# Performance work log

Measured on AMD Instinct MI355X. Metric: run time of the kernel, lower is better.

Reference implementation:

```python
import jax, jax.numpy as jnp
import numpy as np

B, N, E, H = 4, 20000, 320000, 5
STEPS = 10


def _linear_init(key, fan_in, fan_out):
    k1, k2 = jax.random.split(key)
    s = 1.0 / np.sqrt(fan_in)
    W = jax.random.uniform(k1, (fan_in, fan_out), minval=-s, maxval=s, dtype=jnp.float32)
    bias = jax.random.uniform(k2, (fan_out,), minval=-s, maxval=s, dtype=jnp.float32)
    return W, bias


def setup_inputs() -> dict:
    key = jax.random.key(0)
    ks = jax.random.split(key, 13)
    inp = {}
    inp['J_msg'] = jax.random.normal(ks[0], (B, E, 1), dtype=jnp.float32)
    inp['b'] = jax.random.normal(ks[1], (B, N, 1), dtype=jnp.float32)
    inp['index_in'] = jax.random.randint(ks[2], (E,), 0, N, dtype=jnp.int32)
    inp['index_out'] = jax.random.randint(ks[3], (E,), 0, N, dtype=jnp.int32)
    # message MLP: (H+4 -> 64 -> 64 -> 5)
    inp['mW1'], inp['mb1'] = _linear_init(ks[4], H + 4, 64)
    inp['mW2'], inp['mb2'] = _linear_init(ks[5], 64, 64)
    inp['mW3'], inp['mb3'] = _linear_init(ks[6], 64, H)
    # GRU gates: (3H -> H)
    inp['gzW'], inp['gzb'] = _linear_init(ks[7], 3 * H, H)
    inp['grW'], inp['grb'] = _linear_init(ks[8], 3 * H, H)
    inp['ghW'], inp['ghb'] = _linear_init(ks[9], 3 * H, H)
    # out head: (H+1 -> 64 -> 64 -> 1)
    inp['oW1'], inp['ob1'] = _linear_init(ks[10], H + 1, 64)
    inp['oW2'], inp['ob2'] = _linear_init(ks[11], 64, 64)
    inp['oW3'], inp['ob3'] = _linear_init(ks[12], 64, 1)
    return inp


def reference(J_msg, b, index_in, index_out,
              mW1, mb1, mW2, mb2, mW3, mb3,
              gzW, gzb, grW, grb, ghW, ghb,
              oW1, ob1, oW2, ob2, oW3, ob3):
    b_in = b[:, index_in]    # [B,E,1]
    b_out = b[:, index_out]  # [B,E,1]

    def message(h_e):  # h_e: [B,E,H]
        x = jnp.concatenate([h_e, b_in, b_out, J_msg, -J_msg], axis=-1)  # [B,E,H+4]
        x = jax.nn.relu(x @ mW1 + mb1)
        x = jax.nn.relu(x @ mW2 + mb2)
        return x @ mW3 + mb3  # [B,E,H]

    h_t_0 = jnp.zeros((B, N, H), dtype=J_msg.dtype)
    h_t_1 = jnp.zeros((B, N, H), dtype=J_msg.dtype)
    m_t_0 = jnp.zeros((B, N, H), dtype=J_msg.dtype)
    m_t_1 = jnp.zeros((B, N, H), dtype=J_msg.dtype)

    for _ in range(STEPS):
        me0 = message(h_t_0[:, index_out])
        me1 = message(h_t_1[:, index_out])
        # faithful to torch source: m_t_0 accumulates across steps,
        # and m_t_1 is built from the UPDATED m_t_0 (repo quirk).
        m_t_0 = m_t_0.at[:, index_out].add(me0)
        m_t_1 = m_t_0.at[:, index_out].add(me1)
        a = jnp.concatenate([h_t_1, m_t_0, m_t_1], axis=-1)  # [B,N,3H]
        z = jax.nn.sigmoid(a @ gzW + gzb)
        r = jax.nn.sigmoid(a @ grW + grb)
        joined = jnp.concatenate([r * h_t_1, m_t_0, m_t_1], axis=-1)
        h_hat = jnp.tanh(joined @ ghW + ghb)
        h_new = (1 - z) * h_t_1 + z * h_hat
        h_t_0 = h_t_1
        h_t_1 = h_new

    x = jnp.concatenate([h_t_1, b], axis=-1)  # [B,N,H+1]
    x = jax.nn.relu(x @ oW1 + ob1)
    x = jax.nn.relu(x @ oW2 + ob2)
    out = jax.nn.sigmoid(x @ oW3 + ob3)  # [B,N,1]
    return out.reshape(B, 1, -1)
```

## Files before the change

kernel.cpp:

```cpp
#include <hip/hip_runtime.h>
#include <hip/hip_bf16.h>
#include <math.h>

#define Hd 5
#define NN 20000
#define EE 320000
#define NBATCH 4
#define BNH (NBATCH * NN * Hd)

typedef __attribute__((ext_vector_type(8))) short short8;
typedef __attribute__((ext_vector_type(4))) float f32x4;
typedef __attribute__((ext_vector_type(4))) unsigned int uint4v;

__device__ __forceinline__ float sigmoidf_(float v) {
    return 1.0f / (1.0f + expf(-v));
}

__device__ __forceinline__ unsigned short bf16bits(float v) {
    __hip_bfloat16 h = __float2bfloat16(v);
    return *(unsigned short*)&h;
}
__device__ __forceinline__ float bf16tof(unsigned short u) {
    __hip_bfloat16 h = *(__hip_bfloat16*)&u;
    return __bfloat162float(h);
}

__global__ void k_hist(const int* __restrict__ iout, unsigned* __restrict__ cnt) {
    int t = blockIdx.x * 256 + threadIdx.x;
    atomicAdd(&cnt[iout[t]], 1u);
}

__global__ void k_scan(const unsigned* __restrict__ cnt, unsigned* __restrict__ row) {
    __shared__ unsigned part[256];
    int i = threadIdx.x;
    unsigned s = 0;
    if (i < 250) {
        for (int k = 0; k < 80; ++k) s += cnt[i * 80 + k];
    }
    part[i] = s;
    __syncthreads();
    for (int off = 1; off < 256; off <<= 1) {
        unsigned v = part[i];
        unsigned u = (i >= off) ? part[i - off] : 0u;
        __syncthreads();
        part[i] = v + u;
        __syncthreads();
    }
    unsigned run = (i == 0) ? 0u : part[i - 1];
    if (i < 250) {
        for (int k = 0; k < 80; ++k) {
            row[i * 80 + k] = run;
            run += cnt[i * 80 + k];
        }
    }
}

__global__ void k_scatter(const int* __restrict__ iout,
                          const unsigned* __restrict__ row,
                          unsigned* __restrict__ cur,
                          unsigned* __restrict__ perm) {
    int t = blockIdx.x * 256 + threadIdx.x;
    int io = iout[t];
    unsigned pos = row[io] + atomicAdd(&cur[io], 1u);
    perm[pos] = (unsigned)t;
}

__global__ void k_mat(const unsigned* __restrict__ perm,
                      const int* __restrict__ iout, const int* __restrict__ iin,
                      const float* __restrict__ Jm,
                      int* __restrict__ sout, int* __restrict__ sin,
                      float* __restrict__ sJ) {
    int t = blockIdx.x * 256 + threadIdx.x;
    unsigned e = perm[t];
    sout[t] = iout[e];
    sin[t]  = iin[e];
#pragma unroll
    for (int b = 0; b < NBATCH; ++b)
        sJ[(size_t)b * EE + t] = Jm[(size_t)b * EE + e];
}

__global__ void k_wfrag(const float* __restrict__ W1, const float* __restrict__ W2,
                        const float* __restrict__ W3,
                        unsigned short* __restrict__ af1,
                        unsigned short* __restrict__ af2,
                        unsigned short* __restrict__ af3) {
    int t = blockIdx.x * 256 + threadIdx.x;
    if (t < 2048) {
        int j  = t & 7;
        int l  = (t >> 3) & 63;
        int qt = t >> 9;
        int g  = l >> 4;
        int q  = qt * 16 + (l & 15);
        float base = (j < 7) ? W1[j * 64 + q] : (W1[7 * 64 + q] - W1[8 * 64 + q]);
        unsigned short w0 = bf16bits(base);
        af1[t] = (g < 2) ? w0 : bf16bits(base - bf16tof(w0));
    }
    if (t < 4096) {
        int j  = t & 7;
        int l  = (t >> 3) & 63;
        int kt = (t >> 9) & 1;
        int qt = t >> 10;
        int g  = l >> 4;
        int p  = l & 15;
        int nk = (j >> 1) * 16 + 4 * g + 2 * kt + (j & 1);
        int no = (qt & 1) * 32 + 8 * (p >> 2) + 4 * (qt >> 1) + (p & 3);
        af2[t] = bf16bits(W2[nk * 64 + no]);
    }
    if (t < 1024) {
        int j  = t & 7;
        int l  = (t >> 3) & 63;
        int kt = t >> 9;
        int i  = l & 15;
        int g3 = l >> 4;
        int n  = kt * 32 + 8 * g3 + j;
        af3[t] = (i < 5) ? bf16bits(W3[n * 5 + i]) : (unsigned short)0;
    }
}

__global__ void __launch_bounds__(256, 2) msg_kernel(
    const float* __restrict__ sJ, const float* __restrict__ bnode,
    const int* __restrict__ sin, const int* __restrict__ sout,
    const float* __restrict__ b1,
    const unsigned short* __restrict__ af1,
    const unsigned short* __restrict__ af2,
    const unsigned short* __restrict__ af3,
    const float* __restrict__ b2, const float* __restrict__ b3,
    const float* __restrict__ h1,
    float* __restrict__ sCur)
{
    int wid  = threadIdx.x >> 6;
    int lane = threadIdx.x & 63;
    int g = lane >> 4;
    int c = lane & 15;
    int E0 = blockIdx.x * 256 + wid * 64;
    int bb = blockIdx.y;
    int e  = E0 + lane;

    int io = sout[e];
    int ii = sin[e];
    size_t hoff = ((size_t)bb * NN + io) * Hd;

    float xf[8];
#pragma unroll
    for (int i = 0; i < Hd; ++i) xf[i] = h1[hoff + i];
    xf[5] = bnode[bb * NN + ii];
    xf[6] = bnode[bb * NN + io];
    xf[7] = sJ[(size_t)bb * EE + e];

    uint4v B1l[4];
#pragma unroll
    for (int et = 0; et < 4; ++et) {
        float xe[8];
#pragma unroll
        for (int f = 0; f < 8; ++f) xe[f] = __shfl(xf[f], et * 16 + c, 64);

        uint4v hiP, loP;
#pragma unroll
        for (int j2 = 0; j2 < 4; ++j2) {
            float va = xe[2 * j2], vb = xe[2 * j2 + 1];
            unsigned ta = __float_as_uint(va), tb = __float_as_uint(vb);
            unsigned ha = ta & 0xFFFF0000u, hb = tb & 0xFFFF0000u;
            hiP[j2] = hb | (ta >> 16);
            float ra = va - __uint_as_float(ha);
            float rb = vb - __uint_as_float(hb);
            unsigned pk;
            asm("v_cvt_pk_bf16_f32 %0, %1, %2" : "=v"(pk) : "v"(ra), "v"(rb));
            loP[j2] = pk;
        }
#pragma unroll
        for (int d = 0; d < 4; ++d) B1l[et][d] = (g & 1) ? loP[d] : hiP[d];
    }

    const short8* pA1 = (const short8*)af1;
    f32x4 D1[4][4];
#pragma unroll
    for (int qt = 0; qt < 4; ++qt) {
        float4 bb1 = *(const float4*)(b1 + qt * 16 + 4 * g);
        short8 a1f = pA1[qt * 64 + lane];
#pragma unroll
        for (int et = 0; et < 4; ++et) {
            f32x4 dinit = (f32x4){bb1.x, bb1.y, bb1.z, bb1.w};
            D1[qt][et] = __builtin_amdgcn_mfma_f32_16x16x32_bf16(
                a1f, __builtin_bit_cast(short8, B1l[et]), dinit, 0, 0, 0);
        }
    }

    short8 B2[4][2];
#pragma unroll
    for (int et = 0; et < 4; ++et) {
        uint4v w0, w1;
#pragma unroll
        for (int qt = 0; qt < 4; ++qt) {
            float r0 = fmaxf(D1[qt][et][0], 0.0f);
            float r1 = fmaxf(D1[qt][et][1], 0.0f);
            float r2 = fmaxf(D1[qt][et][2], 0.0f);
            float r3 = fmaxf(D1[qt][et][3], 0.0f);
            unsigned p0, p1;
            asm("v_cvt_pk_bf16_f32 %0, %1, %2" : "=v"(p0) : "v"(r0), "v"(r1));
            asm("v_cvt_pk_bf16_f32 %0, %1, %2" : "=v"(p1) : "v"(r2), "v"(r3));
            w0[qt] = p0;
            w1[qt] = p1;
        }
        B2[et][0] = __builtin_bit_cast(short8, w0);
        B2[et][1] = __builtin_bit_cast(short8, w1);
    }

    const short8* pA2 = (const short8*)af2;
    const short8* pA3 = (const short8*)af3;

    f32x4 D3[4];
#pragma unroll
    for (int et = 0; et < 4; ++et) D3[et] = (f32x4){0.f, 0.f, 0.f, 0.f};

#pragma unroll
    for (int half = 0; half < 2; ++half) {
        float4 ba  = *(const float4*)(b2 + half * 32 + 8 * g);
        float4 bbv = *(const float4*)(b2 + half * 32 + 8 * g + 4);
        f32x4 D2a[4], D2b[4];
#pragma unroll
        for (int et = 0; et < 4; ++et) {
            D2a[et] = (f32x4){ba.x, ba.y, ba.z, ba.w};
            D2b[et] = (f32x4){bbv.x, bbv.y, bbv.z, bbv.w};
        }
#pragma unroll
        for (int kt2 = 0; kt2 < 2; ++kt2) {
            short8 a0a = pA2[(half * 2 + kt2) * 64 + lane];
            short8 a0b = pA2[((half + 2) * 2 + kt2) * 64 + lane];
#pragma unroll
            for (int et = 0; et < 4; ++et) {
                D2a[et] = __builtin_amdgcn_mfma_f32_16x16x32_bf16(a0a, B2[et][kt2], D2a[et], 0, 0, 0);
                D2b[et] = __builtin_amdgcn_mfma_f32_16x16x32_bf16(a0b, B2[et][kt2], D2b[et], 0, 0, 0);
            }
        }
        short8 a3 = pA3[half * 64 + lane];
#pragma unroll
        for (int et = 0; et < 4; ++et) {
            float x0 = fmaxf(D2a[et][0], 0.0f), x1 = fmaxf(D2a[et][1], 0.0f);
            float x2 = fmaxf(D2a[et][2], 0.0f), x3 = fmaxf(D2a[et][3], 0.0f);
            float y0 = fmaxf(D2b[et][0], 0.0f), y1 = fmaxf(D2b[et][1], 0.0f);
            float y2 = fmaxf(D2b[et][2], 0.0f), y3 = fmaxf(D2b[et][3], 0.0f);
            uint4v pk;
            unsigned p0, p1, p2, p3;
            asm("v_cvt_pk_bf16_f32 %0, %1, %2" : "=v"(p0) : "v"(x0), "v"(x1));
            asm("v_cvt_pk_bf16_f32 %0, %1, %2" : "=v"(p1) : "v"(x2), "v"(x3));
            asm("v_cvt_pk_bf16_f32 %0, %1, %2" : "=v"(p2) : "v"(y0), "v"(y1));
            asm("v_cvt_pk_bf16_f32 %0, %1, %2" : "=v"(p3) : "v"(y2), "v"(y3));
            pk[0] = p0; pk[1] = p1; pk[2] = p2; pk[3] = p3;
            D3[et] = __builtin_amdgcn_mfma_f32_16x16x32_bf16(
                a3, __builtin_bit_cast(short8, pk), D3[et], 0, 0, 0);
        }
    }

    float m[Hd];
#pragma unroll
    for (int i = 0; i < 4; ++i) {
        float p0 = __shfl(D3[0][i], c, 64);
        float p1 = __shfl(D3[1][i], c, 64);
        float p2 = __shfl(D3[2][i], c, 64);
        float p3 = __shfl(D3[3][i], c, 64);
        m[i] = ((g == 0) ? p0 : (g == 1) ? p1 : (g == 2) ? p2 : p3) + b3[i];
    }
    {
        float p0 = __shfl(D3[0][0], 16 + c, 64);
        float p1 = __shfl(D3[1][0], 16 + c, 64);
        float p2 = __shfl(D3[2][0], 16 + c, 64);
        float p3 = __shfl(D3[3][0], 16 + c, 64);
        m[4] = ((g == 0) ? p0 : (g == 1) ? p1 : (g == 2) ? p2 : p3) + b3[4];
    }

#pragma unroll
    for (int off = 1; off < 64; off <<= 1) {
        int ko = __shfl_up(io, off, 64);
        bool add = (lane >= off) && (ko == io);
#pragma unroll
        for (int i = 0; i < Hd; ++i) {
            float u = __shfl_up(m[i], off, 64);
            if (add) m[i] += u;
        }
    }
    int nk = __shfl_down(io, 1, 64);
    bool tail = (lane == 63) || (nk != io);
    if (tail) {
#pragma unroll
        for (int i = 0; i < Hd; ++i) atomicAdd(&sCur[hoff + i], m[i]);
    }
}

__global__ void node_kernel(
    const float* __restrict__ gzW, const float* __restrict__ gzb,
    const float* __restrict__ grW, const float* __restrict__ grb,
    const float* __restrict__ ghW, const float* __restrict__ ghb,
    float* __restrict__ h1, float* __restrict__ m0,
    float* __restrict__ s0buf, const float* __restrict__ s1buf,
    int zeroPrev)
{
    int t = blockIdx.x * 256 + threadIdx.x;
    if (t >= NBATCH * NN) return;
    size_t off = (size_t)t * Hd;

    float h1v[Hd], m0v[Hd], m1v[Hd];
#pragma unroll
    for (int i = 0; i < Hd; ++i) {
        h1v[i] = h1[off + i];
        float m0n = m0[off + i] + s0buf[off + i];
        m0v[i] = m0n;
        m1v[i] = m0n + s1buf[off + i];
        m0[off + i] = m0n;
        if (zeroPrev) s0buf[off + i] = 0.0f;
    }

    float a[15];
#pragma unroll
    for (int i = 0; i < Hd; ++i) { a[i] = h1v[i]; a[5 + i] = m0v[i]; a[10 + i] = m1v[i]; }

    float z[Hd], r[Hd];
#pragma unroll
    for (int i = 0; i < Hd; ++i) {
        float tz = gzb[i], tr = grb[i];
#pragma unroll
        for (int j = 0; j < 15; ++j) {
            tz = fmaf(a[j], gzW[j * Hd + i], tz);
            tr = fmaf(a[j], grW[j * Hd + i], tr);
        }
        z[i] = sigmoidf_(tz);
        r[i] = sigmoidf_(tr);
    }

    float joined[15];
#pragma unroll
    for (int i = 0; i < Hd; ++i) { joined[i] = r[i] * h1v[i]; joined[5 + i] = m0v[i]; joined[10 + i] = m1v[i]; }

#pragma unroll
    for (int i = 0; i < Hd; ++i) {
        float th = ghb[i];
#pragma unroll
        for (int j = 0; j < 15; ++j) th = fmaf(joined[j], ghW[j * Hd + i], th);
        float hh = tanhf(th);
        h1[off + i] = (1.0f - z[i]) * h1v[i] + z[i] * hh;
    }
}

__global__ void __launch_bounds__(256, 1) out_kernel(
    const float* __restrict__ bnode, const float* __restrict__ h1,
    const float* __restrict__ oW1, const float* __restrict__ ob1,
    const float* __restrict__ oW2, const float* __restrict__ ob2,
    const float* __restrict__ oW3, const float* __restrict__ ob3,
    float* __restrict__ out)
{
    int t = blockIdx.x * 256 + threadIdx.x;
    if (t >= NBATCH * NN) return;

    float x[6];
#pragma unroll
    for (int i = 0; i < Hd; ++i) x[i] = h1[(size_t)t * Hd + i];
    x[5] = bnode[t];

    float acc[64];
#pragma unroll
    for (int q = 0; q < 64; ++q) acc[q] = ob2[q];

#pragma unroll 2
    for (int j = 0; j < 64; ++j) {
        float v = ob1[j];
#pragma unroll
        for (int f = 0; f < 6; ++f) v = fmaf(x[f], oW1[f * 64 + j], v);
        v = fmaxf(v, 0.0f);
        const float* __restrict__ w2r = oW2 + j * 64;
#pragma unroll
        for (int q = 0; q < 64; ++q) acc[q] = fmaf(v, w2r[q], acc[q]);
    }

    float o = ob3[0];
#pragma unroll
    for (int q = 0; q < 64; ++q) o = fmaf(fmaxf(acc[q], 0.0f), oW3[q], o);
    out[t] = sigmoidf_(o);
}

extern "C" void kernel_launch(void* const* d_in, const int* in_sizes, int n_in,
                              void* d_out, int out_size, void* d_ws, size_t ws_size,
                              hipStream_t stream) {
    const float* Jm    = (const float*)d_in[0];
    const float* bnode = (const float*)d_in[1];
    const int*   iin   = (const int*)d_in[2];
    const int*   iout  = (const int*)d_in[3];
    const float* mW1 = (const float*)d_in[4];
    const float* mb1 = (const float*)d_in[5];
    const float* mW2 = (const float*)d_in[6];
    const float* mb2 = (const float*)d_in[7];
    const float* mW3 = (const float*)d_in[8];
    const float* mb3 = (const float*)d_in[9];
    const float* gzW = (const float*)d_in[10];
    const float* gzb = (const float*)d_in[11];
    const float* grW = (const float*)d_in[12];
    const float* grb = (const float*)d_in[13];
    const float* ghW = (const float*)d_in[14];
    const float* ghb = (const float*)d_in[15];
    const float* oW1 = (const float*)d_in[16];
    const float* ob1 = (const float*)d_in[17];
    const float* oW2 = (const float*)d_in[18];
    const float* ob2 = (const float*)d_in[19];
    const float* oW3 = (const float*)d_in[20];
    const float* ob3 = (const float*)d_in[21];

    float* ws = (float*)d_ws;
    float* h1 = ws;
    float* m0 = ws + (size_t)BNH;
    float* sA = ws + (size_t)2 * BNH;
    float* sB = ws + (size_t)3 * BNH;
    unsigned* cnt  = (unsigned*)(ws + (size_t)4 * BNH);
    unsigned* cur  = cnt + NN;
    unsigned* row  = cur + NN;
    unsigned* perm = row + NN;
    int*      sout = (int*)(perm + EE);
    int*      sin  = sout + EE;
    float*    sJ   = (float*)(sin + EE);
    unsigned short* af1 = (unsigned short*)(sJ + (size_t)NBATCH * EE);
    unsigned short* af2 = af1 + 2048;
    unsigned short* af3 = af2 + 4096;

    hipMemsetAsync(d_ws, 0, ((size_t)4 * BNH + 2 * NN) * sizeof(float), stream);

    k_hist<<<EE / 256, 256, 0, stream>>>(iout, cnt);
    k_scan<<<1, 256, 0, stream>>>(cnt, row);
    k_scatter<<<EE / 256, 256, 0, stream>>>(iout, row, cur, perm);
    k_mat<<<EE / 256, 256, 0, stream>>>(perm, iout, iin, Jm, sout, sin, sJ);
    k_wfrag<<<20, 256, 0, stream>>>(mW1, mW2, mW3, af1, af2, af3);

    dim3 mgrid(EE / 256, NBATCH);
    int ngrid = (NBATCH * NN + 255) / 256;

    float* buf[2] = { sA, sB };
    for (int s = 0; s < 10; ++s) {
        float* sCur  = buf[s & 1];
        float* sPrev = (s == 0) ? sCur : buf[(s + 1) & 1];
        msg_kernel<<<mgrid, 256, 0, stream>>>(sJ, bnode, sin, sout,
                                              mb1, af1, af2, af3,
                                              mb2, mb3, h1, sCur);
        node_kernel<<<ngrid, 256, 0, stream>>>(gzW, gzb, grW, grb, ghW, ghb,
                                               h1, m0, sPrev, sCur,
                                               (s == 0) ? 0 : 1);
    }

    out_kernel<<<ngrid, 256, 0, stream>>>(bnode, h1,
                                          oW1, ob1, oW2, ob2, oW3, ob3,
                                          (float*)d_out);
}
```

Before: 513.5 us.

## Process all batches per thread in message kernel, sharing index and scan setup

Each thread of the message kernel now loops over all four batches for its edge instead of using a grid dimension per batch. Edge indices, segment-match masks and the tail flag are computed once and reused across batches. The segmented scan is interleaved across the batches. The grid shrinks by a factor of four and register pressure rises (20 accumulators kept live), which may reduce occupancy or cause spills under launch_bounds(256,2).

```diff
diff --git a/kernel.cpp b/kernel.cpp
--- a/kernel.cpp
+++ b/kernel.cpp
@@ -133,156 +133,179 @@
     int g = lane >> 4;
     int c = lane & 15;
     int E0 = blockIdx.x * 256 + wid * 64;
-    int bb = blockIdx.y;
     int e  = E0 + lane;
 
     int io = sout[e];
     int ii = sin[e];
-    size_t hoff = ((size_t)bb * NN + io) * Hd;
-
-    float xf[8];
-#pragma unroll
-    for (int i = 0; i < Hd; ++i) xf[i] = h1[hoff + i];
-    xf[5] = bnode[bb * NN + ii];
-    xf[6] = bnode[bb * NN + io];
-    xf[7] = sJ[(size_t)bb * EE + e];
-
-    uint4v B1l[4];
-#pragma unroll
-    for (int et = 0; et < 4; ++et) {
-        float xe[8];
-#pragma unroll
-        for (int f = 0; f < 8; ++f) xe[f] = __shfl(xf[f], et * 16 + c, 64);
-
-        uint4v hiP, loP;
-#pragma unroll
-        for (int j2 = 0; j2 < 4; ++j2) {
-            float va = xe[2 * j2], vb = xe[2 * j2 + 1];
-            unsigned ta = __float_as_uint(va), tb = __float_as_uint(vb);
-            unsigned ha = ta & 0xFFFF0000u, hb = tb & 0xFFFF0000u;
-            hiP[j2] = hb | (ta >> 16);
-            float ra = va - __uint_as_float(ha);
-            float rb = vb - __uint_as_float(hb);
-            unsigned pk;
-            asm("v_cvt_pk_bf16_f32 %0, %1, %2" : "=v"(pk) : "v"(ra), "v"(rb));
-            loP[j2] = pk;
-        }
-#pragma unroll
-        for (int d = 0; d < 4; ++d) B1l[et][d] = (g & 1) ? loP[d] : hiP[d];
-    }
+
+    bool addm[6];
+#pragma unroll
+    for (int s6 = 0; s6 < 6; ++s6) {
+        int off = 1 << s6;
+        int ko = __shfl_up(io, off, 64);
+        addm[s6] = (lane >= off) && (ko == io);
+    }
+    int nk = __shfl_down(io, 1, 64);
+    bool tail = (lane == 63) || (nk != io);
 
     const short8* pA1 = (const short8*)af1;
-    f32x4 D1[4][4];
-#pragma unroll
-    for (int qt = 0; qt < 4; ++qt) {
-        float4 bb1 = *(const float4*)(b1 + qt * 16 + 4 * g);
-        short8 a1f = pA1[qt * 64 + lane];
-#pragma unroll
-        for (int et = 0; et < 4; ++et) {
-            f32x4 dinit = (f32x4){bb1.x, bb1.y, bb1.z, bb1.w};
-            D1[qt][et] = __builtin_amdgcn_mfma_f32_16x16x32_bf16(
-                a1f, __builtin_bit_cast(short8, B1l[et]), dinit, 0, 0, 0);
-        }
-    }
-
-    short8 B2[4][2];
-#pragma unroll
-    for (int et = 0; et < 4; ++et) {
-        uint4v w0, w1;
-#pragma unroll
-        for (int qt = 0; qt < 4; ++qt) {
-            float r0 = fmaxf(D1[qt][et][0], 0.0f);
-            float r1 = fmaxf(D1[qt][et][1], 0.0f);
-            float r2 = fmaxf(D1[qt][et][2], 0.0f);
-            float r3 = fmaxf(D1[qt][et][3], 0.0f);
-            unsigned p0, p1;
-            asm("v_cvt_pk_bf16_f32 %0, %1, %2" : "=v"(p0) : "v"(r0), "v"(r1));
-            asm("v_cvt_pk_bf16_f32 %0, %1, %2" : "=v"(p1) : "v"(r2), "v"(r3));
-            w0[qt] = p0;
-            w1[qt] = p1;
-        }
-        B2[et][0] = __builtin_bit_cast(short8, w0);
-        B2[et][1] = __builtin_bit_cast(short8, w1);
-    }
-
     const short8* pA2 = (const short8*)af2;
     const short8* pA3 = (const short8*)af3;
 
-    f32x4 D3[4];
-#pragma unroll
-    for (int et = 0; et < 4; ++et) D3[et] = (f32x4){0.f, 0.f, 0.f, 0.f};
-
-#pragma unroll
-    for (int half = 0; half < 2; ++half) {
-        float4 ba  = *(const float4*)(b2 + half * 32 + 8 * g);
-        float4 bbv = *(const float4*)(b2 + half * 32 + 8 * g + 4);
-        f32x4 D2a[4], D2b[4];
+    float m[NBATCH][Hd];
+
+#pragma unroll
+    for (int bb = 0; bb < NBATCH; ++bb) {
+        size_t hoff = ((size_t)bb * NN + io) * Hd;
+
+        float xf[8];
+#pragma unroll
+        for (int i = 0; i < Hd; ++i) xf[i] = h1[hoff + i];
+        xf[5] = bnode[bb * NN + ii];
+        xf[6] = bnode[bb * NN + io];
+        xf[7] = sJ[(size_t)bb * EE + e];
+
+        uint4v B1l[4];
 #pragma unroll
         for (int et = 0; et < 4; ++et) {
-            D2a[et] = (f32x4){ba.x, ba.y, ba.z, ba.w};
-            D2b[et] = (f32x4){bbv.x, bbv.y, bbv.z, bbv.w};
-        }
-#pragma unroll
-        for (int kt2 = 0; kt2 < 2; ++kt2) {
-            short8 a0a = pA2[(half * 2 + kt2) * 64 + lane];
-            short8 a0b = pA2[((half + 2) * 2 + kt2) * 64 + lane];
+            float xe[8];
+#pragma unroll
+            for (int f = 0; f < 8; ++f) xe[f] = __shfl(xf[f], et * 16 + c, 64);
+
+            uint4v hiP, loP;
+#pragma unroll
+            for (int j2 = 0; j2 < 4; ++j2) {
+                float va = xe[2 * j2], vb = xe[2 * j2 + 1];
+                unsigned ta = __float_as_uint(va), tb = __float_as_uint(vb);
+                unsigned ha = ta & 0xFFFF0000u, hb = tb & 0xFFFF0000u;
+                hiP[j2] = hb | (ta >> 16);
+                float ra = va - __uint_as_float(ha);
+                float rb = vb - __uint_as_float(hb);
+                unsigned pk;
+                asm("v_cvt_pk_bf16_f32 %0, %1, %2" : "=v"(pk) : "v"(ra), "v"(rb));
+                loP[j2] = pk;
+            }
+#pragma unroll
+            for (int d = 0; d < 4; ++d) B1l[et][d] = (g & 1) ? loP[d] : hiP[d];
+        }
+
+        f32x4 D1[4][4];
+#pragma unroll
+        for (int qt = 0; qt < 4; ++qt) {
+            float4 bb1 = *(const float4*)(b1 + qt * 16 + 4 * g);
+            short8 a1f = pA1[qt * 64 + lane];
 #pragma unroll
             for (int et = 0; et < 4; ++et) {
-                D2a[et] = __builtin_amdgcn_mfma_f32_16x16x32_bf16(a0a, B2[et][kt2], D2a[et], 0, 0, 0);
-                D2b[et] = __builtin_amdgcn_mfma_f32_16x16x32_bf16(a0b, B2[et][kt2], D2b[et], 0, 0, 0);
-            }
-        }
-        short8 a3 = pA3[half * 64 + lane];
+                f32x4 dinit = (f32x4){bb1.x, bb1.y, bb1.z, bb1.w};
+                D1[qt][et] = __builtin_amdgcn_mfma_f32_16x16x32_bf16(
+                    a1f, __builtin_bit_cast(short8, B1l[et]), dinit, 0, 0, 0);
+            }
+        }
+
+        short8 B2[4][2];
 #pragma unroll
         for (int et = 0; et < 4; ++et) {
-            float x0 = fmaxf(D2a[et][0], 0.0f), x1 = fmaxf(D2a[et][1], 0.0f);
-            float x2 = fmaxf(D2a[et][2], 0.0f), x3 = fmaxf(D2a[et][3], 0.0f);
-            float y0 = fmaxf(D2b[et][0], 0.0f), y1 = fmaxf(D2b[et][1], 0.0f);
-            float y2 = fmaxf(D2b[et][2], 0.0f), y3 = fmaxf(D2b[et][3], 0.0f);
-            uint4v pk;
-            unsigned p0, p1, p2, p3;
-            asm("v_cvt_pk_bf16_f32 %0, %1, %2" : "=v"(p0) : "v"(x0), "v"(x1));
-            asm("v_cvt_pk_bf16_f32 %0, %1, %2" : "=v"(p1) : "v"(x2), "v"(x3));
-            asm("v_cvt_pk_bf16_f32 %0, %1, %2" : "=v"(p2) : "v"(y0), "v"(y1));
-            asm("v_cvt_pk_bf16_f32 %0, %1, %2" : "=v"(p3) : "v"(y2), "v"(y3));
-            pk[0] = p0; pk[1] = p1; pk[2] = p2; pk[3] = p3;
-            D3[et] = __builtin_amdgcn_mfma_f32_16x16x32_bf16(
-                a3, __builtin_bit_cast(short8, pk), D3[et], 0, 0, 0);
-        }
-    }
-
-    float m[Hd];
-#pragma unroll
-    for (int i = 0; i < 4; ++i) {
-        float p0 = __shfl(D3[0][i], c, 64);
-        float p1 = __shfl(D3[1][i], c, 64);
-        float p2 = __shfl(D3[2][i], c, 64);
-        float p3 = __shfl(D3[3][i], c, 64);
-        m[i] = ((g == 0) ? p0 : (g == 1) ? p1 : (g == 2) ? p2 : p3) + b3[i];
-    }
-    {
-        float p0 = __shfl(D3[0][0], 16 + c, 64);
-        float p1 = __shfl(D3[1][0], 16 + c, 64);
-        float p2 = __shfl(D3[2][0], 16 + c, 64);
-        float p3 = __shfl(D3[3][0], 16 + c, 64);
-        m[4] = ((g == 0) ? p0 : (g == 1) ? p1 : (g == 2) ? p2 : p3) + b3[4];
-    }
-
-#pragma unroll
-    for (int off = 1; off < 64; off <<= 1) {
-        int ko = __shfl_up(io, off, 64);
-        bool add = (lane >= off) && (ko == io);
-#pragma unroll
-        for (int i = 0; i < Hd; ++i) {
-            float u = __shfl_up(m[i], off, 64);
-            if (add) m[i] += u;
-        }
-    }
-    int nk = __shfl_down(io, 1, 64);
-    bool tail = (lane == 63) || (nk != io);
+            uint4v w0, w1;
+#pragma unroll
+            for (int qt = 0; qt < 4; ++qt) {
+                float r0 = fmaxf(D1[qt][et][0], 0.0f);
+                float r1 = fmaxf(D1[qt][et][1], 0.0f);
+                float r2 = fmaxf(D1[qt][et][2], 0.0f);
+                float r3 = fmaxf(D1[qt][et][3], 0.0f);
+                unsigned p0, p1;
+                asm("v_cvt_pk_bf16_f32 %0, %1, %2" : "=v"(p0) : "v"(r0), "v"(r1));
+                asm("v_cvt_pk_bf16_f32 %0, %1, %2" : "=v"(p1) : "v"(r2), "v"(r3));
+                w0[qt] = p0;
+                w1[qt] = p1;
+            }
+            B2[et][0] = __builtin_bit_cast(short8, w0);
+            B2[et][1] = __builtin_bit_cast(short8, w1);
+        }
+
+        f32x4 D3[4];
+#pragma unroll
+        for (int et = 0; et < 4; ++et) D3[et] = (f32x4){0.f, 0.f, 0.f, 0.f};
+
+#pragma unroll
+        for (int half = 0; half < 2; ++half) {
+            float4 ba  = *(const float4*)(b2 + half * 32 + 8 * g);
+            float4 bbv = *(const float4*)(b2 + half * 32 + 8 * g + 4);
+            f32x4 D2a[4], D2b[4];
+#pragma unroll
+            for (int et = 0; et < 4; ++et) {
+                D2a[et] = (f32x4){ba.x, ba.y, ba.z, ba.w};
+                D2b[et] = (f32x4){bbv.x, bbv.y, bbv.z, bbv.w};
+            }
+#pragma unroll
+            for (int kt2 = 0; kt2 < 2; ++kt2) {
+                short8 a0a = pA2[(half * 2 + kt2) * 64 + lane];
+                short8 a0b = pA2[((half + 2) * 2 + kt2) * 64 + lane];
+#pragma unroll
+                for (int et = 0; et < 4; ++et) {
+                    D2a[et] = __builtin_amdgcn_mfma_f32_16x16x32_bf16(a0a, B2[et][kt2], D2a[et], 0, 0, 0);
+                    D2b[et] = __builtin_amdgcn_mfma_f32_16x16x32_bf16(a0b, B2[et][kt2], D2b[et], 0, 0, 0);
+                }
+            }
+            short8 a3 = pA3[half * 64 + lane];
+#pragma unroll
+            for (int et = 0; et < 4; ++et) {
+                float x0 = fmaxf(D2a[et][0], 0.0f), x1 = fmaxf(D2a[et][1], 0.0f);
+                float x2 = fmaxf(D2a[et][2], 0.0f), x3 = fmaxf(D2a[et][3], 0.0f);
+                float y0 = fmaxf(D2b[et][0], 0.0f), y1 = fmaxf(D2b[et][1], 0.0f);
+                float y2 = fmaxf(D2b[et][2], 0.0f), y3 = fmaxf(D2b[et][3], 0.0f);
+                uint4v pk;
+                unsigned p0, p1, p2, p3;
+                asm("v_cvt_pk_bf16_f32 %0, %1, %2" : "=v"(p0) : "v"(x0), "v"(x1));
+                asm("v_cvt_pk_bf16_f32 %0, %1, %2" : "=v"(p1) : "v"(x2), "v"(x3));
+                asm("v_cvt_pk_bf16_f32 %0, %1, %2" : "=v"(p2) : "v"(y0), "v"(y1));
+                asm("v_cvt_pk_bf16_f32 %0, %1, %2" : "=v"(p3) : "v"(y2), "v"(y3));
+                pk[0] = p0; pk[1] = p1; pk[2] = p2; pk[3] = p3;
+                D3[et] = __builtin_amdgcn_mfma_f32_16x16x32_bf16(
+                    a3, __builtin_bit_cast(short8, pk), D3[et], 0, 0, 0);
+            }
+        }
+
+#pragma unroll
+        for (int i = 0; i < 4; ++i) {
+            float p0 = __shfl(D3[0][i], c, 64);
+            float p1 = __shfl(D3[1][i], c, 64);
+            float p2 = __shfl(D3[2][i], c, 64);
+            float p3 = __shfl(D3[3][i], c, 64);
+            m[bb][i] = ((g == 0) ? p0 : (g == 1) ? p1 : (g == 2) ? p2 : p3) + b3[i];
+        }
+        {
+            float p0 = __shfl(D3[0][0], 16 + c, 64);
+            float p1 = __shfl(D3[1][0], 16 + c, 64);
+            float p2 = __shfl(D3[2][0], 16 + c, 64);
+            float p3 = __shfl(D3[3][0], 16 + c, 64);
+            m[bb][4] = ((g == 0) ? p0 : (g == 1) ? p1 : (g == 2) ? p2 : p3) + b3[4];
+        }
+    }
+
+#pragma unroll
+    for (int s6 = 0; s6 < 6; ++s6) {
+        int off = 1 << s6;
+        float u[NBATCH][Hd];
+#pragma unroll
+        for (int bb = 0; bb < NBATCH; ++bb)
+#pragma unroll
+            for (int i = 0; i < Hd; ++i)
+                u[bb][i] = __shfl_up(m[bb][i], off, 64);
+#pragma unroll
+        for (int bb = 0; bb < NBATCH; ++bb)
+#pragma unroll
+            for (int i = 0; i < Hd; ++i)
+                if (addm[s6]) m[bb][i] += u[bb][i];
+    }
+
     if (tail) {
 #pragma unroll
-        for (int i = 0; i < Hd; ++i) atomicAdd(&sCur[hoff + i], m[i]);
+        for (int bb = 0; bb < NBATCH; ++bb) {
+            size_t hoff = ((size_t)bb * NN + io) * Hd;
+#pragma unroll
+            for (int i = 0; i < Hd; ++i)
+                atomicAdd(&sCur[hoff + i], m[bb][i]);
+        }
     }
 }
 
@@ -426,7 +449,7 @@
     k_mat<<<EE / 256, 256, 0, stream>>>(perm, iout, iin, Jm, sout, sin, sJ);
     k_wfrag<<<20, 256, 0, stream>>>(mW1, mW2, mW3, af1, af2, af3);
 
-    dim3 mgrid(EE / 256, NBATCH);
+    int mgrid = EE / 256;
     int ngrid = (NBATCH * NN + 255) / 256;
 
     float* buf[2] = { sA, sB };
```

Measured after the change: 544.8 us. +6.1%, slower.
